# Kernel tuning notes

Measured on AMD Instinct MI355X. Metric: run time of the kernel, lower is better.

Reference implementation:

```python
import jax, jax.numpy as jnp
import numpy as np

NB, DM, DIN, DS, DTR, K = 4, 64, 128, 16, 4, 4
C, COUT, H, W, BATCH, NH = 256, 256, 32, 32, 4, 8


def layernorm(x, w, b, eps=1e-5):
    mu = x.mean(-1, keepdims=True)
    var = ((x - mu) ** 2).mean(-1, keepdims=True)
    return (x - mu) * jax.lax.rsqrt(var + eps) * w + b


def ln_hw(x, eps=1e-5):
    # F.layer_norm(x, [H, W]) -> normalize over last two dims, no affine
    mu = x.mean((-2, -1), keepdims=True)
    var = ((x - mu) ** 2).mean((-2, -1), keepdims=True)
    return (x - mu) * jax.lax.rsqrt(var + eps)


def conv1d(x, w, b, groups=1, pad=1):
    # x: (B, Cin, L), w: (Cout, Cin//groups, k)
    y = jax.lax.conv_general_dilated(x, w, (1,), [(pad, pad)],
                                     dimension_numbers=('NCH', 'OIH', 'NCH'),
                                     feature_group_count=groups)
    return y + b[None, :, None]


def selective_scan(u, dt, Bm, Cm, A, Dp):
    # u, dt: (B,L,din); Bm, Cm: (B,L,ds); A: (din,ds); Dp: (din,)
    dA = jnp.exp(dt[..., None] * A)                     # (B,L,din,ds)
    dBu = (dt * u)[..., None] * Bm[:, :, None, :]       # (B,L,din,ds)

    def step(h, inp):
        dA_t, dBu_t, C_t = inp
        h = dA_t * h + dBu_t
        return h, jnp.einsum('bds,bs->bd', h, C_t)

    h0 = jnp.zeros((u.shape[0], DIN, DS), u.dtype)
    _, ys = jax.lax.scan(step, h0, (dA.transpose(1, 0, 2, 3), dBu.transpose(1, 0, 2, 3), Cm.transpose(1, 0, 2)))
    return ys.transpose(1, 0, 2) + u * Dp


def mamba(xs, inw, convw, convb, xpw, dtw, dtb, alog, dp, outw):
    # xs: (B,L,DM) one branch of Mamba(d_model=DM, d_state=DS, d_conv=K, expand=2)
    xz = xs @ inw.T                                     # (B,L,2*DIN)
    u, z = jnp.split(xz, 2, axis=-1)
    # causal depthwise conv1d (torch pads K-1 and truncates to L == left pad K-1)
    uc = jax.lax.conv_general_dilated(u.transpose(0, 2, 1), convw[:, None, :], (1,), [(K - 1, 0)],
                                      dimension_numbers=('NCH', 'OIH', 'NCH'),
                                      feature_group_count=DIN) + convb[None, :, None]
    u = jax.nn.silu(uc.transpose(0, 2, 1))              # (B,L,DIN)
    xdbc = u @ xpw.T                                    # (B,L,DTR+2*DS)
    dt = jax.nn.softplus(xdbc[..., :DTR] @ dtw.T + dtb)
    Bm, Cm = xdbc[..., DTR:DTR + DS], xdbc[..., DTR + DS:]
    y = selective_scan(u, dt, Bm, Cm, -jnp.exp(alog), dp)
    return (y * jax.nn.silu(z)) @ outw.T


mamba_v = jax.vmap(mamba)  # over branch axis 0 of inputs and all params


def mha(x, inw, inb, outw, outb):
    B, N, Cc = x.shape
    hd = Cc // NH
    qkv = x @ inw.T + inb
    q, k, v = jnp.split(qkv, 3, axis=-1)
    q = q.reshape(B, N, NH, hd).transpose(0, 2, 1, 3)
    k = k.reshape(B, N, NH, hd).transpose(0, 2, 1, 3)
    v = v.reshape(B, N, NH, hd).transpose(0, 2, 1, 3)
    att = jax.nn.softmax((q @ k.transpose(0, 1, 3, 2)) * (1.0 / (hd ** 0.5)), axis=-1)
    o = (att @ v).transpose(0, 2, 1, 3).reshape(B, N, Cc)
    return o @ outw.T + outb


def reference(x, norm_w, norm_b, skip_scale, m_inw, m_convw, m_convb, m_xpw, m_dtw, m_dtb, m_alog, m_d, m_outw, qdw_w, qdw_b, qpw_w, qpw_b, rdw_w, rdw_b, rpw_w, rpw_b, fdw_w, fdw_b, fpw_w, fpw_b, lc_w, lc_b, attn_inw, attn_inb, attn_outw, attn_outb, lgn_w, lgn_b, fc_w, fc_b, dwc_w, dwc_b, proj_w, proj_b):
    B, Cc, Hh, Ww = x.shape
    N = Hh * Ww
    xs = x.reshape(B, Cc, N).transpose(0, 2, 1)         # (B,N,C)
    xn = layernorm(xs, norm_w, norm_b)
    # channel-chunk into NB branches: (NB,B,N,DM)
    xc = xn.reshape(B, N, NB, DM).transpose(2, 0, 1, 3)
    xm = mamba_v(xc, m_inw, m_convw, m_convb, m_xpw, m_dtw, m_dtb, m_alog, m_d, m_outw) + skip_scale * xc
    x_concat = xm.transpose(1, 2, 0, 3).reshape(B, N, Cc)
    # branch gating: depthwise grouped conv (C->NB) then pointwise (NB->NB)
    Q = conv1d(conv1d(x_concat.transpose(0, 2, 1), qdw_w, qdw_b, groups=NB, pad=1), qpw_w, qpw_b, groups=1, pad=0)
    g = jax.nn.sigmoid(Q)                               # (B,NB,N)
    xg = (g.transpose(1, 0, 2)[..., None] * xm).transpose(1, 2, 0, 3).reshape(B, N, Cc)
    xgt = xg.transpose(0, 2, 1)                          # (B,C,N)
    R = conv1d(conv1d(xgt, rdw_w, rdw_b, groups=Cc, pad=1), rpw_w, rpw_b, groups=1, pad=0) + xgt
    cat = jnp.concatenate([xs, R.transpose(0, 2, 1)], axis=-1).transpose(0, 2, 1)  # (B,2C,N)
    xm2 = conv1d(conv1d(cat, fdw_w, fdw_b, groups=2 * Cc, pad=1), fpw_w, fpw_b, groups=1, pad=0) + cat[:, :Cc, :]
    xm2 = xm2.transpose(0, 2, 1)                         # (B,N,C)
    # local-global feature mixing
    x_local = conv1d(xm2.transpose(0, 2, 1), lc_w, lc_b, groups=Cc, pad=1).transpose(0, 2, 1)
    x_global = mha(xm2, attn_inw, attn_inb, attn_outw, attn_outb)
    x_out = jnp.concatenate([x_local, x_global], axis=-1) @ fc_w.T + fc_b
    x_out = jax.nn.gelu(layernorm(x_out, lgn_w, lgn_b), approximate=False)
    # DepthwiseConvolution: layer_norm over [H,W] (no affine) then depthwise conv2d
    xi = x_out.transpose(0, 2, 1).reshape(B, Cc, Hh, Ww)
    xi = ln_hw(xi)
    xi = jax.lax.conv_general_dilated(xi, dwc_w, (1, 1), [(1, 1), (1, 1)],
                                      dimension_numbers=('NCHW', 'OIHW', 'NCHW'),
                                      feature_group_count=Cc) + dwc_b[None, :, None, None]
    x_mixed = xi.reshape(B, Cc, N).transpose(0, 2, 1)
    x_mixed = layernorm(x_mixed, norm_w, norm_b)        # self.norm reused
    x_mixed = x_mixed @ proj_w.T + proj_b
    return x_mixed.transpose(0, 2, 1).reshape(B, COUT, Hh, Ww)


def setup_inputs() -> dict:
    key = jax.random.key(0)
    ks = iter(jax.random.split(key, 64))

    def rn(shape, s=0.02):
        return jax.random.normal(next(ks), shape, jnp.float32) * s

    return dict(
        x=jax.random.normal(next(ks), (BATCH, C, H, W), jnp.float32),
        norm_w=jnp.ones((C,), jnp.float32), norm_b=jnp.zeros((C,), jnp.float32),
        skip_scale=jnp.ones((1,), jnp.float32),
        m_inw=rn((NB, 2 * DIN, DM)), m_convw=rn((NB, DIN, K), 0.2), m_convb=jnp.zeros((NB, DIN), jnp.float32),
        m_xpw=rn((NB, DTR + 2 * DS, DIN)), m_dtw=rn((NB, DIN, DTR), 0.2), m_dtb=rn((NB, DIN), 0.5),
        m_alog=jnp.tile(jnp.log(jnp.arange(1, DS + 1, dtype=jnp.float32)), (NB, DIN, 1)),
        m_d=jnp.ones((NB, DIN), jnp.float32), m_outw=rn((NB, DM, DIN)),
        qdw_w=rn((NB, C // NB, 3), 0.1), qdw_b=jnp.zeros((NB,), jnp.float32),
        qpw_w=rn((NB, NB, 1), 0.3), qpw_b=jnp.zeros((NB,), jnp.float32),
        rdw_w=rn((C, 1, 3), 0.2), rdw_b=jnp.zeros((C,), jnp.float32),
        rpw_w=rn((C, C, 1)), rpw_b=jnp.zeros((C,), jnp.float32),
        fdw_w=rn((2 * C, 1, 3), 0.2), fdw_b=jnp.zeros((2 * C,), jnp.float32),
        fpw_w=rn((C, 2 * C, 1)), fpw_b=jnp.zeros((C,), jnp.float32),
        lc_w=rn((C, 1, 3), 0.2), lc_b=jnp.zeros((C,), jnp.float32),
        attn_inw=rn((3 * C, C)), attn_inb=jnp.zeros((3 * C,), jnp.float32),
        attn_outw=rn((C, C)), attn_outb=jnp.zeros((C,), jnp.float32),
        lgn_w=jnp.ones((C,), jnp.float32), lgn_b=jnp.zeros((C,), jnp.float32),
        fc_w=rn((C, 2 * C)), fc_b=jnp.zeros((C,), jnp.float32),
        dwc_w=rn((C, 1, 3, 3), 0.2), dwc_b=jnp.zeros((C,), jnp.float32),
        proj_w=rn((COUT, C)), proj_b=jnp.zeros((COUT,), jnp.float32),
    )
```

## Files before the change

### kernel.cpp

```cpp
#include <hip/hip_runtime.h>
#include <math.h>


namespace {
constexpr int NB_ = 4, DM_ = 64, DIN_ = 128, DS_ = 16, DTR_ = 4;
constexpr int C_ = 256, N_ = 1024, B_ = 4, HD_ = 32;
constexpr int NCH = 16, LCH = 64;
constexpr int NSTATE = 16 * 128 * 16;
}

typedef __attribute__((ext_vector_type(8))) short bf16x8;
typedef __attribute__((ext_vector_type(4))) float f32x4;
typedef __attribute__((ext_vector_type(8))) unsigned short ushort8v;
typedef __attribute__((ext_vector_type(4))) unsigned short ushort4v;

__device__ __forceinline__ unsigned short f2b(float f) {
  unsigned int u = __float_as_uint(f);
  unsigned int r = u + 0x7FFFu + ((u >> 16) & 1u);
  return (unsigned short)(r >> 16);
}

__device__ __forceinline__ float2 blockReduce2(float a, float b, float* red) {
#pragma unroll
  for (int m = 1; m < 64; m <<= 1) {
// ... 64 lines not shown
__global__ __launch_bounds__(256) void k_inproj_mfma(const float* __restrict__ xn,
                                                     const float* __restrict__ inw,
                                                     float* __restrict__ UPRE,
                                                     float* __restrict__ Z) {
  __shared__ unsigned short xa[64][72];
  __shared__ unsigned short wb[64][72];
  int r0 = blockIdx.x * 64;
  int nb = blockIdx.y >> 2, c0 = (blockIdx.y & 3) * 64;
  int t = threadIdx.x;
  int wv = t >> 6, lane = t & 63, g = lane >> 4, ql = lane & 15;
  const f32x4 zf = {0.f, 0.f, 0.f, 0.f};
  f32x4 acc[4] = {zf, zf, zf, zf};
  int rr = t >> 2, kq = (t & 3) * 16;
  {
    const float* xsrc = xn + (long)(r0 + rr) * C_ + nb * 64 + kq;
#pragma unroll
    for (int j = 0; j < 4; ++j) {
      float4 v = *(const float4*)(xsrc + 4 * j);
      ushort4v u = {f2b(v.x), f2b(v.y), f2b(v.z), f2b(v.w)};
      *(ushort4v*)&xa[rr][kq + 4 * j] = u;
    }
    const float* wsrc = inw + ((long)nb * 256 + c0 + rr) * 64 + kq;
#pragma unroll
    for (int j = 0; j < 4; ++j) {
      float4 v = *(const float4*)(wsrc + 4 * j);
      ushort4v u = {f2b(v.x), f2b(v.y), f2b(v.z), f2b(v.w)};
      *(ushort4v*)&wb[rr][kq + 4 * j] = u;
    }
  }
  __syncthreads();
#pragma unroll
  for (int ks = 0; ks < 2; ++ks) {
    bf16x8 a = *(const bf16x8*)&xa[wv * 16 + ql][ks * 32 + g * 8];
#pragma unroll
    for (int ct = 0; ct < 4; ++ct) {
      bf16x8 b = *(const bf16x8*)&wb[ct * 16 + ql][ks * 32 + g * 8];
      acc[ct] = __builtin_amdgcn_mfma_f32_16x16x32_bf16(a, b, acc[ct], 0, 0, 0);
    }
  }
#pragma unroll
  for (int ct = 0; ct < 4; ++ct) {
    int col = c0 + ct * 16 + ql;
#pragma unroll
    for (int reg = 0; reg < 4; ++reg) {
      long row = (long)nb * 4096 + r0 + wv * 16 + g * 4 + reg;
      if (col < 128) UPRE[row * DIN_ + col] = acc[ct][reg];
      else           Z[row * DIN_ + col - 128] = acc[ct][reg];
    }
  }
}

__global__ __launch_bounds__(256) void k_causal(const float* __restrict__ Uin,
                                                float* __restrict__ Uout,
                                                const float* __restrict__ cw,
                                                const float* __restrict__ cb) {
  __shared__ float u_s[35][128];
  int bx = blockIdx.x;
  int nbb = bx >> 5, chk = bx & 31;
  int nb = nbb >> 2;
  int n0 = chk * 32;
  const float* ibase = Uin + (long)nbb * N_ * DIN_;
  float* obase = Uout + (long)nbb * N_ * DIN_;
  for (int i = threadIdx.x; i < 35 * 32; i += 256) {
    int row = i >> 5, q = i & 31;
    int n = n0 - 3 + row;
    float4 v = (n >= 0) ? *(const float4*)&ibase[(long)n * DIN_ + q * 4]
                        : make_float4(0.f, 0.f, 0.f, 0.f);
    *(float4*)&u_s[row][q * 4] = v;
  }
  __syncthreads();
  int d = threadIdx.x & 127, half = threadIdx.x >> 7;
  float w0 = cw[(nb * DIN_ + d) * 4 + 0], w1 = cw[(nb * DIN_ + d) * 4 + 1];
  float w2 = cw[(nb * DIN_ + d) * 4 + 2], w3 = cw[(nb * DIN_ + d) * 4 + 3];
  float bv = cb[nb * DIN_ + d];
#pragma unroll
  for (int j = 0; j < 16; ++j) {
    int nn = half * 16 + j;
    float acc = bv + w3 * u_s[nn + 3][d] + w2 * u_s[nn + 2][d] +
                w1 * u_s[nn + 1][d] + w0 * u_s[nn][d];
    obase[(long)(n0 + nn) * DIN_ + d] = siluf(acc);
  }
}

__global__ __launch_bounds__(256) void k_xdbc(const float* __restrict__ U,
                                              const float* __restrict__ xpw,
                                              const float* __restrict__ dtw,
                                              const float* __restrict__ dtb,
                                              float* __restrict__ DT,
                                              float* __restrict__ BMb, float* __restrict__ CMb) {
  __shared__ float wl[36][129];
  __shared__ float u16[16][129];
  __shared__ float xd_s[16][37];
  __shared__ float dtw_s[128][4];
  __shared__ float dtb_s[128];
  int t = threadIdx.x;
  long row0 = (long)blockIdx.x * 16;
  int nb = blockIdx.x >> 8;
  for (int i = t; i < 36 * 128; i += 256) wl[i >> 7][i & 127] = xpw[nb * 36 * 128 + i];
  for (int i = t; i < 16 * 128; i += 256) u16[i >> 7][i & 127] = U[(row0 + (i >> 7)) * DIN_ + (i & 127)];
  for (int i = t; i < 512; i += 256) dtw_s[i >> 2][i & 3] = dtw[nb * 512 + i];
  if (t < 128) dtb_s[t] = dtb[nb * DIN_ + t];
  __syncthreads();
  {
    int r = t >> 4, jl = t & 15;
    float a0 = 0.f, a1 = 0.f, a2 = 0.f;
    for (int k = 0; k < 128; ++k) {
      float uv = u16[r][k];
      a0 += uv * wl[jl][k];
      a1 += uv * wl[jl + 16][k];
      if (jl < 4) a2 += uv * wl[jl + 32][k];
    }
    xd_s[r][jl] = a0;
    xd_s[r][jl + 16] = a1;
    if (jl < 4) xd_s[r][jl + 32] = a2;
  }
  __syncthreads();
  {
    int r = t >> 4, s = t & 15;
    BMb[(row0 + r) * DS_ + s] = xd_s[r][4 + s];
    CMb[(row0 + r) * DS_ + s] = xd_s[r][20 + s];
  }
  {
    int r = t >> 4, dl = t & 15;
    float x0 = xd_s[r][0], x1 = xd_s[r][1], x2 = xd_s[r][2], x3 = xd_s[r][3];
#pragma unroll
    for (int dd = 0; dd < 8; ++dd) {
      int d = dl * 8 + dd;
      float a = dtb_s[d] + x0 * dtw_s[d][0] + x1 * dtw_s[d][1] +
                x2 * dtw_s[d][2] + x3 * dtw_s[d][3];
      DT[(row0 + r) * DIN_ + d] = softplusf(a);
    }
  }
}

__global__ __launch_bounds__(256) void k_scanA(const float* __restrict__ DT,
                                               const float* __restrict__ U,
                                               const float* __restrict__ BMb,
                                               const float* __restrict__ alog,
                                               float* __restrict__ Aprod,
                                               float* __restrict__ Hend) {
  __shared__ float dt_s[64][64];
  __shared__ float u_s[64][64];
  __shared__ float bm_s[64][16];
  int bx = blockIdx.x;
  int chunk = bx >> 5, rem = bx & 31, nbb = rem >> 1, dh = rem & 1;
  int nb = nbb >> 2;
  int t = threadIdx.x;
  int dl = t >> 2, sg = t & 3;
  int d = dh * 64 + dl;
  long base = (long)nbb * N_ + chunk * LCH;
#pragma unroll
  for (int j = 0; j < 4; ++j) {
    int f = t + 256 * j;
    int tt = f >> 4, dq = (f & 15) * 4;
    long src = (base + tt) * DIN_ + dh * 64 + dq;
    *(float4*)&dt_s[tt][dq] = *(const float4*)&DT[src];
    *(float4*)&u_s[tt][dq]  = *(const float4*)&U[src];
  }
  {
    int tt = t >> 2, sq = (t & 3) * 4;
    *(float4*)&bm_s[tt][sq] = *(const float4*)&BMb[(base + tt) * DS_ + sq];
  }
  float A[4];
#pragma unroll
  for (int i = 0; i < 4; ++i)
    A[i] = -expf(alog[(nb * DIN_ + d) * DS_ + sg * 4 + i]);
  __syncthreads();
  float h[4] = {0.f, 0.f, 0.f, 0.f};
  float ap[4] = {1.f, 1.f, 1.f, 1.f};
  for (int tt = 0; tt < LCH; ++tt) {
    float dtv = dt_s[tt][dl];
    float uv  = u_s[tt][dl];
    float cc = dtv * uv;
    float4 bm4 = *(const float4*)&bm_s[tt][sg * 4];
    float bmv[4] = {bm4.x, bm4.y, bm4.z, bm4.w};
#pragma unroll
    for (int i = 0; i < 4; ++i) {
      float dA = __expf(dtv * A[i]);
      h[i] = dA * h[i] + cc * bmv[i];
      ap[i] *= dA;
    }
  }
  long st = (long)chunk * NSTATE + ((nbb << 7) + d) * 16 + sg * 4;
  *(float4*)&Aprod[st] = make_float4(ap[0], ap[1], ap[2], ap[3]);
  *(float4*)&Hend[st]  = make_float4(h[0], h[1], h[2], h[3]);
}

__global__ __launch_bounds__(256) void k_scanB(float* __restrict__ Aprod,
                                               const float* __restrict__ Hend) {
  int state = blockIdx.x * 256 + threadIdx.x;
  float H = 0.f;
#pragma unroll
  for (int c = 0; c < NCH; ++c) {
    long idx = (long)c * NSTATE + state;
    float a = Aprod[idx];
    float e = Hend[idx];
    Aprod[idx] = H;
    H = e + a * H;
  }
}

__global__ __launch_bounds__(256) void k_scanC(float* __restrict__ DT,
                                               const float* __restrict__ U,
                                               const float* __restrict__ BMb,
                                               const float* __restrict__ CMb,
                                               const float* __restrict__ alog,
                                               const float* __restrict__ Dp,
                                               const float* __restrict__ Hin) {
  __shared__ float dt_s[64][64];
  __shared__ float u_s[64][64];
  __shared__ float bm_s[64][16];
  __shared__ float cm_s[64][16];
  int bx = blockIdx.x;
// ... 170 lines not shown
  }
}

template <int KD>
__global__ __launch_bounds__(256) void k_gemm_cm_dw(const float* __restrict__ inA,
                                                    const float* __restrict__ inB,
                                                    const float* __restrict__ dww,
                                                    const float* __restrict__ dwb,
                                                    const float* __restrict__ w,
                                                    const float* __restrict__ bias,
                                                    const float* __restrict__ residCM,
                                                    const float* __restrict__ residRM,
                                                    float* __restrict__ outCM,
                                                    float* __restrict__ outRM) {
  __shared__ unsigned short xa[64][72];
  __shared__ unsigned short wb[64][72];
  int rb = blockIdx.x;
  int b = rb >> 4, n0 = (rb & 15) * 64;
  int c0 = blockIdx.y * 64;
  int t = threadIdx.x;
  int wv = t >> 6, lane = t & 63, g = lane >> 4, ql = lane & 15;
  const f32x4 zf = {0.f, 0.f, 0.f, 0.f};
  f32x4 acc[4] = {zf, zf, zf, zf};
  int rr = t >> 2, kq = (t & 3) * 16;
  for (int k0 = 0; k0 < KD; k0 += 64) {
    __syncthreads();
    {
      int k = k0 + rr;
      const float* src = (inB != nullptr && k >= 256)
                             ? inB + ((long)(b * 256 + k - 256)) * 1024
                             : inA + ((long)(b * 256 + k)) * 1024;
      float w0 = dww[k * 3], w1 = dww[k * 3 + 1], w2 = dww[k * 3 + 2], bv = dwb[k];
#pragma unroll
      for (int j = 0; j < 4; ++j) {
        int nb4 = n0 + kq + 4 * j;
        float4 v = *(const float4*)&src[nb4];
        float vm1 = (nb4 > 0) ? src[nb4 - 1] : 0.f;
        float vp4 = (nb4 + 4 < 1024) ? src[nb4 + 4] : 0.f;
        xa[kq + 4 * j + 0][rr] = f2b(bv + w0 * vm1 + w1 * v.x + w2 * v.y);
        xa[kq + 4 * j + 1][rr] = f2b(bv + w0 * v.x + w1 * v.y + w2 * v.z);
        xa[kq + 4 * j + 2][rr] = f2b(bv + w0 * v.y + w1 * v.z + w2 * v.w);
        xa[kq + 4 * j + 3][rr] = f2b(bv + w0 * v.z + w1 * v.w + w2 * vp4);
      }
    }
    const float* wsrc = w + (long)(c0 + rr) * KD + k0 + kq;
#pragma unroll
    for (int j = 0; j < 4; ++j) {
      float4 v = *(const float4*)(wsrc + 4 * j);
      ushort4v u = {f2b(v.x), f2b(v.y), f2b(v.z), f2b(v.w)};
      *(ushort4v*)&wb[rr][kq + 4 * j] = u;
    }
    __syncthreads();
#pragma unroll
    for (int ks = 0; ks < 2; ++ks) {
      bf16x8 a = *(const bf16x8*)&xa[wv * 16 + ql][ks * 32 + g * 8];
#pragma unroll
      for (int ct = 0; ct < 4; ++ct) {
        bf16x8 bfr = *(const bf16x8*)&wb[ct * 16 + ql][ks * 32 + g * 8];
        acc[ct] = __builtin_amdgcn_mfma_f32_16x16x32_bf16(a, bfr, acc[ct], 0, 0, 0);
      }
    }
  }
#pragma unroll
  for (int ct = 0; ct < 4; ++ct) {
    int col = c0 + ct * 16 + ql;
    float bv = bias[col];
    if (outCM) {
      long base = ((long)(b * 256 + col)) * 1024 + n0 + wv * 16 + g * 4;
      float4 r4 = *(const float4*)(residCM + base);
      float4 o = make_float4(acc[ct][0] + bv + r4.x, acc[ct][1] + bv + r4.y,
                             acc[ct][2] + bv + r4.z, acc[ct][3] + bv + r4.w);
      *(float4*)(outCM + base) = o;
    } else {
#pragma unroll
      for (int reg = 0; reg < 4; ++reg) {
        long row = (long)b * 1024 + n0 + wv * 16 + g * 4 + reg;
        long idx = row * 256 + col;
        outRM[idx] = acc[ct][reg] + bv + residRM[idx];
      }
    }
  }
}

template <int KD, bool TOUT>
__global__ __launch_bounds__(256) void k_gemm_rm(const float* __restrict__ inA,
                                                 const float* __restrict__ inB,
                                                 const float* __restrict__ w,
                                                 const float* __restrict__ bias,
                                                 float* __restrict__ out,
                                                 int Cout, int lda) {
  __shared__ unsigned short xa[64][72];
  __shared__ unsigned short wb[64][72];
  __shared__ float tt[TOUT ? 64 : 1][TOUT ? 68 : 1];
  int r0 = blockIdx.x * 64;
  int c0 = blockIdx.y * 64;
  int t = threadIdx.x;
  int wv = t >> 6, lane = t & 63, g = lane >> 4, ql = lane & 15;
  const f32x4 zf = {0.f, 0.f, 0.f, 0.f};
  f32x4 acc[4] = {zf, zf, zf, zf};
  int rr = t >> 2, kq = (t & 3) * 16;
  for (int k0 = 0; k0 < KD; k0 += 64) {
    __syncthreads();
    int kk = k0 + kq;
    const float* xsrc = (inB != nullptr && kk >= KD / 2)
                            ? inB + (long)(r0 + rr) * lda + (kk - KD / 2)
                            : inA + (long)(r0 + rr) * lda + kk;
#pragma unroll
    for (int j = 0; j < 4; ++j) {
      float4 v = *(const float4*)(xsrc + 4 * j);
      ushort4v u = {f2b(v.x), f2b(v.y), f2b(v.z), f2b(v.w)};
      *(ushort4v*)&xa[rr][kq + 4 * j] = u;
    }
    const float* wsrc = w + (long)(c0 + rr) * KD + kk;
#pragma unroll
    for (int j = 0; j < 4; ++j) {
      float4 v = *(const float4*)(wsrc + 4 * j);
      ushort4v u = {f2b(v.x), f2b(v.y), f2b(v.z), f2b(v.w)};
      *(ushort4v*)&wb[rr][kq + 4 * j] = u;
    }
    __syncthreads();
#pragma unroll
    for (int ks = 0; ks < 2; ++ks) {
      bf16x8 a = *(const bf16x8*)&xa[wv * 16 + ql][ks * 32 + g * 8];
#pragma unroll
      for (int ct = 0; ct < 4; ++ct) {
        bf16x8 b = *(const bf16x8*)&wb[ct * 16 + ql][ks * 32 + g * 8];
        acc[ct] = __builtin_amdgcn_mfma_f32_16x16x32_bf16(a, b, acc[ct], 0, 0, 0);
      }
    }
  }
  if constexpr (!TOUT) {
#pragma unroll
    for (int ct = 0; ct < 4; ++ct) {
      int col = c0 + ct * 16 + ql;
      float bv = bias[col];
#pragma unroll
      for (int reg = 0; reg < 4; ++reg) {
        long row = r0 + wv * 16 + g * 4 + reg;
        out[row * Cout + col] = acc[ct][reg] + bv;
      }
    }
  } else {
#pragma unroll
    for (int ct = 0; ct < 4; ++ct) {
      int col = ct * 16 + ql;
      float bv = bias[c0 + col];
#pragma unroll
      for (int reg = 0; reg < 4; ++reg)
        tt[col][wv * 16 + g * 4 + reg] = acc[ct][reg] + bv;
    }
    __syncthreads();
    int b = r0 >> 10, n0 = r0 & 1023;
    int col = t >> 2, nq = (t & 3) * 16;
    float* op = out + ((long)(b * 256 + c0 + col)) * 1024 + n0 + nq;
#pragma unroll
    for (int j = 0; j < 4; ++j) {
      float4 v = make_float4(tt[col][nq + 4 * j], tt[col][nq + 4 * j + 1],
                             tt[col][nq + 4 * j + 2], tt[col][nq + 4 * j + 3]);
      *(float4*)(op + 4 * j) = v;
    }
  }
}

__global__ __launch_bounds__(256) void k_gemm_qkv(const float* __restrict__ in,
                                                  const float* __restrict__ w,
                                                  const float* __restrict__ bias,
                                                  unsigned short* __restrict__ out) {
  __shared__ unsigned short xa[64][72];
  __shared__ unsigned short wb[64][72];
  int r0 = blockIdx.x * 64;
  int c0 = blockIdx.y * 64;
  int t = threadIdx.x;
  int wv = t >> 6, lane = t & 63, g = lane >> 4, ql = lane & 15;
  const f32x4 zf = {0.f, 0.f, 0.f, 0.f};
  f32x4 acc[4] = {zf, zf, zf, zf};
  int rr = t >> 2, kq = (t & 3) * 16;
  for (int k0 = 0; k0 < 256; k0 += 64) {
    __syncthreads();
    const float* xsrc = in + (long)(r0 + rr) * 256 + k0 + kq;
#pragma unroll
    for (int j = 0; j < 4; ++j) {
      float4 v = *(const float4*)(xsrc + 4 * j);
      ushort4v u = {f2b(v.x), f2b(v.y), f2b(v.z), f2b(v.w)};
      *(ushort4v*)&xa[rr][kq + 4 * j] = u;
    }
    const float* wsrc = w + (long)(c0 + rr) * 256 + k0 + kq;
#pragma unroll
    for (int j = 0; j < 4; ++j) {
      float4 v = *(const float4*)(wsrc + 4 * j);
      ushort4v u = {f2b(v.x), f2b(v.y), f2b(v.z), f2b(v.w)};
      *(ushort4v*)&wb[rr][kq + 4 * j] = u;
    }
    __syncthreads();
#pragma unroll
    for (int ks = 0; ks < 2; ++ks) {
      bf16x8 a = *(const bf16x8*)&xa[wv * 16 + ql][ks * 32 + g * 8];
#pragma unroll
      for (int ct = 0; ct < 4; ++ct) {
        bf16x8 b = *(const bf16x8*)&wb[ct * 16 + ql][ks * 32 + g * 8];
        acc[ct] = __builtin_amdgcn_mfma_f32_16x16x32_bf16(a, b, acc[ct], 0, 0, 0);
      }
    }
  }
#pragma unroll
  for (int ct = 0; ct < 4; ++ct) {
    int col = c0 + ct * 16 + ql;
    float bv = bias[col];
#pragma unroll
    for (int reg = 0; reg < 4; ++reg) {
      long row = r0 + wv * 16 + g * 4 + reg;
      out[row * 768 + col] = f2b(acc[ct][reg] + bv);
    }
  }
}

__global__ __launch_bounds__(256) void k_gemm_fc(const float* __restrict__ XM2,
                                                 const float* __restrict__ XGL,
                                                 const float* __restrict__ lcw,
                                                 const float* __restrict__ lcb,
                                                 const float* __restrict__ w,
                                                 const float* __restrict__ bias,
                                                 float* __restrict__ out) {
  __shared__ unsigned short xa[64][72];
  __shared__ unsigned short wb[64][72];
  int r0 = blockIdx.x * 64;
  int c0 = blockIdx.y * 64;
  int t = threadIdx.x;
  int wv = t >> 6, lane = t & 63, g = lane >> 4, ql = lane & 15;
  const f32x4 zf = {0.f, 0.f, 0.f, 0.f};
  f32x4 acc[4] = {zf, zf, zf, zf};
  int rr = t >> 2, kq = (t & 3) * 16;
  for (int k0 = 0; k0 < 512; k0 += 64) {
    __syncthreads();
    int kk = k0 + kq;
    long row = r0 + rr;
    if (kk < 256) {
      int n = (int)(row & 1023);
      const float* pc = XM2 + row * 256 + kk;
      bool hm = n > 0, hp = n < 1023;
#pragma unroll
      for (int j = 0; j < 4; ++j) {
        float4 v = *(const float4*)(pc + 4 * j);
// ... 145 lines not shown
  int b = bx >> 6, n0 = (bx & 63) * 16;
  int c = threadIdx.x;
#pragma unroll
  for (int j = 0; j < 16; ++j)
    tile[c][j] = XO[((long)(b * N_ + n0 + j)) * C_ + c];
  __syncthreads();
  {
    int n = c & 15, g = c >> 4;
    float a = 0.f, q = 0.f;
#pragma unroll
    for (int i = 0; i < 16; ++i) {
      float v = tile[g * 16 + i][n];
      a += v; q += v * v;
    }
    redp[g][n][0] = a; redp[g][n][1] = q;
  }
  __syncthreads();
  if (c < 16) {
    float a = 0.f, q = 0.f;
#pragma unroll
    for (int g2 = 0; g2 < 16; ++g2) { a += redp[g2][c][0]; q += redp[g2][c][1]; }
    float mu = a * (1.f / C_);
    float rs = rsqrtf(q * (1.f / C_) - mu * mu + 1e-5f);
    stats[c][0] = mu; stats[c][1] = rs;
  }
  __syncthreads();
  float wv = lw[c], bv = lb[c];
  float o[16];
#pragma unroll
  for (int j = 0; j < 16; ++j) {
    float x = (tile[c][j] - stats[j][0]) * stats[j][1] * wv + bv;
    o[j] = 0.5f * x * (1.f + erff(x * 0.70710678118654752f));
  }
  float* dst = &XI[((long)(b * C_ + c)) * N_ + n0];
#pragma unroll
  for (int j4 = 0; j4 < 4; ++j4)
    *(float4*)(dst + j4 * 4) = make_float4(o[4 * j4], o[4 * j4 + 1], o[4 * j4 + 2], o[4 * j4 + 3]);
}

__global__ __launch_bounds__(256) void k_lnhw_dwc(const float* __restrict__ XIin,
                                                  const float* __restrict__ w,
                                                  const float* __restrict__ bias,
                                                  float* __restrict__ XD) {
  __shared__ float pl[32][33];
  __shared__ float red[8];
  long base = (long)blockIdx.x * 1024;
  int c = blockIdx.x & 255;
  int t = threadIdx.x;
  float4 v = *(const float4*)&XIin[base + t * 4];
  float a = v.x + v.y + v.z + v.w;
  float q = v.x * v.x + v.y * v.y + v.z * v.z + v.w * v.w;
  float2 s = blockReduce2(a, q, red);
  float mu = s.x * (1.f / 1024.f);
  float rs = rsqrtf(s.y * (1.f / 1024.f) - mu * mu + 1e-5f);
  int hh = t >> 3, w0 = (t & 7) * 4;
  pl[hh][w0 + 0] = (v.x - mu) * rs;
  pl[hh][w0 + 1] = (v.y - mu) * rs;
  pl[hh][w0 + 2] = (v.z - mu) * rs;
  pl[hh][w0 + 3] = (v.w - mu) * rs;
  __syncthreads();
  float wk[9];
#pragma unroll
  for (int i = 0; i < 9; ++i) wk[i] = w[c * 9 + i];
  float bv = bias[c];
  float o[4];
#pragma unroll
  for (int j = 0; j < 4; ++j) {
    int ww = w0 + j;
    float acc = bv;
#pragma unroll
    for (int kh = 0; kh < 3; ++kh) {
      int h2 = hh + kh - 1;
      if (h2 < 0 || h2 >= 32) continue;
#pragma unroll
      for (int kw = 0; kw < 3; ++kw) {
        int w2 = ww + kw - 1;
        if (w2 < 0 || w2 >= 32) continue;
        acc += wk[kh * 3 + kw] * pl[h2][w2];
      }
    }
    o[j] = acc;
  }
  *(float4*)&XD[base + t * 4] = make_float4(o[0], o[1], o[2], o[3]);
}

extern "C" void kernel_launch(void* const* d_in, const int* in_sizes, int n_in,
                              void* d_out, int out_size, void* d_ws, size_t ws_size,
                              hipStream_t stream) {
  const float* x        = (const float*)d_in[0];
  const float* norm_w   = (const float*)d_in[1];
  const float* norm_b   = (const float*)d_in[2];
  const float* skip     = (const float*)d_in[3];
  const float* m_inw    = (const float*)d_in[4];
  const float* m_convw  = (const float*)d_in[5];
  const float* m_convb  = (const float*)d_in[6];
  const float* m_xpw    = (const float*)d_in[7];
  const float* m_dtw    = (const float*)d_in[8];
  const float* m_dtb    = (const float*)d_in[9];
  const float* m_alog   = (const float*)d_in[10];
  const float* m_d      = (const float*)d_in[11];
  const float* m_outw   = (const float*)d_in[12];
  const float* qdw_w    = (const float*)d_in[13];
  const float* qdw_b    = (const float*)d_in[14];
  const float* qpw_w    = (const float*)d_in[15];
  const float* qpw_b    = (const float*)d_in[16];
  const float* rdw_w    = (const float*)d_in[17];
  const float* rdw_b    = (const float*)d_in[18];
  const float* rpw_w    = (const float*)d_in[19];
  const float* rpw_b    = (const float*)d_in[20];
  const float* fdw_w    = (const float*)d_in[21];
  const float* fdw_b    = (const float*)d_in[22];
  const float* fpw_w    = (const float*)d_in[23];
  const float* fpw_b    = (const float*)d_in[24];
  const float* lc_w     = (const float*)d_in[25];
  const float* lc_b     = (const float*)d_in[26];
  const float* attn_inw = (const float*)d_in[27];
  const float* attn_inb = (const float*)d_in[28];
  const float* attn_outw= (const float*)d_in[29];
  const float* attn_outb= (const float*)d_in[30];
  const float* lgn_w    = (const float*)d_in[31];
  const float* lgn_b    = (const float*)d_in[32];
  const float* fc_w     = (const float*)d_in[33];
  const float* fc_b     = (const float*)d_in[34];
  const float* dwc_w    = (const float*)d_in[35];
  const float* dwc_b    = (const float*)d_in[36];
  const float* proj_w   = (const float*)d_in[37];
  const float* proj_b   = (const float*)d_in[38];
  float* out = (float*)d_out;

  float* ws = (float*)d_ws;
  const size_t F = 1048576;
  float* XS  = ws + 0 * F;
  float* XN  = ws + 1 * F;
  float* U   = ws + 2 * F;
  float* Z   = ws + 4 * F;
  float* UPRE= ws + 6 * F;
  float* DT  = ws + 6 * F;
  float* BM  = ws + 8 * F;
  float* CM  = ws + 8 * F + F / 4;
  float* XMC = ws + 8 * F + F / 2;
  float* SC_APROD = ws + 8 * F + F / 2;
  float* SC_HEND  = ws + 9 * F;
  float* G   = ws + 1 * F;
  float* XG  = ws + 2 * F;
  float* RB  = ws + 4 * F;
  float* XM2 = ws + 5 * F;
  unsigned short* QKVB = (unsigned short*)(ws + 1 * F);
  float* O   = ws + 4 * F;
  float* XGL = ws + 6 * F;
  float* XO  = ws + 7 * F;
  float* XI  = ws + 8 * F;
  float* XD  = ws + 5 * F;
  float* LNF = ws + 0 * F;
  (void)ws_size; (void)in_sizes; (void)n_in; (void)out_size;

  k_ln_t2<<<256, 256, 0, stream>>>(x, norm_w, norm_b, XN, XS);
  k_inproj_mfma<<<dim3(64, 16), 256, 0, stream>>>(XN, m_inw, UPRE, Z);
  k_causal<<<512, 256, 0, stream>>>(UPRE, U, m_convw, m_convb);
  k_xdbc<<<1024, 256, 0, stream>>>(U, m_xpw, m_dtw, m_dtb, DT, BM, CM);
  k_scanA<<<512, 256, 0, stream>>>(DT, U, BM, m_alog, SC_APROD, SC_HEND);
  k_scanB<<<128, 256, 0, stream>>>(SC_APROD, SC_HEND);
  k_scanC<<<512, 256, 0, stream>>>(DT, U, BM, CM, m_alog, m_d, SC_APROD);
  k_outproj_mfma<<<dim3(64, 4), 256, 0, stream>>>(DT, Z, m_outw, XN, skip, XMC);
  k_gate<<<256, 256, 0, stream>>>(XMC, qdw_w, qdw_b, qpw_w, qpw_b, G);
  k_xg<<<256, 256, 0, stream>>>(XMC, G, XG);
  k_gemm_cm_dw<256><<<dim3(64, 4), 256, 0, stream>>>(XG, nullptr, rdw_w, rdw_b,
                                                     rpw_w, rpw_b, XG, nullptr, RB, nullptr);
  k_gemm_cm_dw<512><<<dim3(64, 4), 256, 0, stream>>>(x, RB, fdw_w, fdw_b,
                                                     fpw_w, fpw_b, nullptr, XS, nullptr, XM2);
  k_gemm_qkv<<<dim3(64, 12), 256, 0, stream>>>(XM2, attn_inw, attn_inb, QKVB);
  k_attn_mfma<<<512, 256, 0, stream>>>(QKVB, O);
  k_gemm_rm<256, false><<<dim3(64, 4), 256, 0, stream>>>(O, nullptr, attn_outw, attn_outb, XGL, 256, 256);
  k_gemm_fc<<<dim3(64, 4), 256, 0, stream>>>(XM2, XGL, lc_w, lc_b, fc_w, fc_b, XO);
  k_lngelu<<<256, 256, 0, stream>>>(XO, lgn_w, lgn_b, XI);
  k_lnhw_dwc<<<1024, 256, 0, stream>>>(XI, dwc_w, dwc_b, XD);
  k_ln_t2<<<256, 256, 0, stream>>>(XD, norm_w, norm_b, LNF, nullptr);
  k_gemm_rm<256, true><<<dim3(64, 4), 256, 0, stream>>>(LNF, nullptr, proj_w, proj_b, out, 256, 256);
}
```

Baseline: 215.3 us.

## Use MFMA for x_proj GEMM and fuse final layernorm into projection

Replaces the scalar FP32 x_proj kernel with a bf16 MFMA tiled GEMM that handles 64 rows per block and writes its outputs as vector stores. Separately, fuses the final token layernorm into the output projection GEMM: each block computes per-token statistics from the channel-major input and normalizes while staging to LDS. This removes one kernel launch and the round trip of the intermediate LNF buffer through global memory. In exchange, x_proj now runs in bf16, the layernorm statistics are recomputed by each of the four column blocks, and the variance uses the one-pass sum-of-squares form, which can lose precision.

```diff
diff --git a/kernel.cpp b/kernel.cpp
--- a/kernel.cpp
+++ b/kernel.cpp
@@ -170,53 +170,96 @@
   }
 }
 
-__global__ __launch_bounds__(256) void k_xdbc(const float* __restrict__ U,
-                                              const float* __restrict__ xpw,
-                                              const float* __restrict__ dtw,
-                                              const float* __restrict__ dtb,
-                                              float* __restrict__ DT,
-                                              float* __restrict__ BMb, float* __restrict__ CMb) {
-  __shared__ float wl[36][129];
-  __shared__ float u16[16][129];
-  __shared__ float xd_s[16][37];
+__global__ __launch_bounds__(256) void k_xdbc_mfma(const float* __restrict__ U,
+                                                   const float* __restrict__ xpw,
+                                                   const float* __restrict__ dtw,
+                                                   const float* __restrict__ dtb,
+                                                   float* __restrict__ DT,
+                                                   float* __restrict__ BMb,
+                                                   float* __restrict__ CMb) {
+  __shared__ unsigned short xa[64][72];
+  __shared__ unsigned short wb[48][72];
+  __shared__ float xd_s[64][40];
   __shared__ float dtw_s[128][4];
   __shared__ float dtb_s[128];
   int t = threadIdx.x;
-  long row0 = (long)blockIdx.x * 16;
-  int nb = blockIdx.x >> 8;
-  for (int i = t; i < 36 * 128; i += 256) wl[i >> 7][i & 127] = xpw[nb * 36 * 128 + i];
-  for (int i = t; i < 16 * 128; i += 256) u16[i >> 7][i & 127] = U[(row0 + (i >> 7)) * DIN_ + (i & 127)];
+  long row0 = (long)blockIdx.x * 64;
+  int nb = blockIdx.x >> 6;
   for (int i = t; i < 512; i += 256) dtw_s[i >> 2][i & 3] = dtw[nb * 512 + i];
   if (t < 128) dtb_s[t] = dtb[nb * DIN_ + t];
+  int wv = t >> 6, lane = t & 63, g = lane >> 4, ql = lane & 15;
+  const f32x4 zf = {0.f, 0.f, 0.f, 0.f};
+  f32x4 acc[3] = {zf, zf, zf};
+  int rr = t >> 2, kq = (t & 3) * 16;
+  for (int k0 = 0; k0 < 128; k0 += 64) {
+    __syncthreads();
+    const float* xsrc = U + (row0 + rr) * DIN_ + k0 + kq;
+#pragma unroll
+    for (int j = 0; j < 4; ++j) {
+      float4 v = *(const float4*)(xsrc + 4 * j);
+      ushort4v u = {f2b(v.x), f2b(v.y), f2b(v.z), f2b(v.w)};
+      *(ushort4v*)&xa[rr][kq + 4 * j] = u;
+    }
+    if (rr < 48) {
+      if (rr < 36) {
+        const float* wsrc = xpw + (long)nb * 36 * 128 + rr * 128 + k0 + kq;
+#pragma unroll
+        for (int j = 0; j < 4; ++j) {
+          float4 v = *(const float4*)(wsrc + 4 * j);
+          ushort4v u = {f2b(v.x), f2b(v.y), f2b(v.z), f2b(v.w)};
+          *(ushort4v*)&wb[rr][kq + 4 * j] = u;
+        }
+      } else {
+        ushort4v z = {0, 0, 0, 0};
+#pragma unroll
+        for (int j = 0; j < 4; ++j) *(ushort4v*)&wb[rr][kq + 4 * j] = z;
+      }
+    }
+    __syncthreads();
+#pragma unroll
+    for (int ks = 0; ks < 2; ++ks) {
+      bf16x8 a = *(const bf16x8*)&xa[wv * 16 + ql][ks * 32 + g * 8];
+#pragma unroll
+      for (int ct = 0; ct < 3; ++ct) {
+        bf16x8 b = *(const bf16x8*)&wb[ct * 16 + ql][ks * 32 + g * 8];
+        acc[ct] = __builtin_amdgcn_mfma_f32_16x16x32_bf16(a, b, acc[ct], 0, 0, 0);
+      }
+    }
+  }
+#pragma unroll
+  for (int ct = 0; ct < 3; ++ct) {
+    int col = ct * 16 + ql;
+    if (col < 36) {
+#pragma unroll
+      for (int reg = 0; reg < 4; ++reg)
+        xd_s[wv * 16 + g * 4 + reg][col] = acc[ct][reg];
+    }
+  }
   __syncthreads();
   {
-    int r = t >> 4, jl = t & 15;
-    float a0 = 0.f, a1 = 0.f, a2 = 0.f;
-    for (int k = 0; k < 128; ++k) {
-      float uv = u16[r][k];
-      a0 += uv * wl[jl][k];
-      a1 += uv * wl[jl + 16][k];
-      if (jl < 4) a2 += uv * wl[jl + 32][k];
-    }
-    xd_s[r][jl] = a0;
-    xd_s[r][jl + 16] = a1;
-    if (jl < 4) xd_s[r][jl + 32] = a2;
-  }
-  __syncthreads();
+    int r = t >> 2, sq = (t & 3) * 4;
+    float4 bm4 = make_float4(xd_s[r][4 + sq], xd_s[r][5 + sq],
+                             xd_s[r][6 + sq], xd_s[r][7 + sq]);
+    *(float4*)&BMb[(row0 + r) * DS_ + sq] = bm4;
+    float4 cm4 = make_float4(xd_s[r][20 + sq], xd_s[r][21 + sq],
+                             xd_s[r][22 + sq], xd_s[r][23 + sq]);
+    *(float4*)&CMb[(row0 + r) * DS_ + sq] = cm4;
+  }
   {
-    int r = t >> 4, s = t & 15;
-    BMb[(row0 + r) * DS_ + s] = xd_s[r][4 + s];
-    CMb[(row0 + r) * DS_ + s] = xd_s[r][20 + s];
-  }
-  {
-    int r = t >> 4, dl = t & 15;
+    int r = t >> 2, dg = t & 3;
     float x0 = xd_s[r][0], x1 = xd_s[r][1], x2 = xd_s[r][2], x3 = xd_s[r][3];
-#pragma unroll
-    for (int dd = 0; dd < 8; ++dd) {
-      int d = dl * 8 + dd;
-      float a = dtb_s[d] + x0 * dtw_s[d][0] + x1 * dtw_s[d][1] +
-                x2 * dtw_s[d][2] + x3 * dtw_s[d][3];
-      DT[(row0 + r) * DIN_ + d] = softplusf(a);
+    float* dst = DT + (row0 + r) * DIN_ + dg * 32;
+#pragma unroll
+    for (int j = 0; j < 8; ++j) {
+      float o[4];
+#pragma unroll
+      for (int e = 0; e < 4; ++e) {
+        int d = dg * 32 + j * 4 + e;
+        float a = dtb_s[d] + x0 * dtw_s[d][0] + x1 * dtw_s[d][1] +
+                  x2 * dtw_s[d][2] + x3 * dtw_s[d][3];
+        o[e] = softplusf(a);
+      }
+      *(float4*)(dst + j * 4) = make_float4(o[0], o[1], o[2], o[3]);
     }
   }
 }
@@ -553,16 +596,13 @@
   }
 }
 
-template <int KD, bool TOUT>
+template <int KD>
 __global__ __launch_bounds__(256) void k_gemm_rm(const float* __restrict__ inA,
-                                                 const float* __restrict__ inB,
                                                  const float* __restrict__ w,
                                                  const float* __restrict__ bias,
-                                                 float* __restrict__ out,
-                                                 int Cout, int lda) {
+                                                 float* __restrict__ out, int Cout) {
   __shared__ unsigned short xa[64][72];
   __shared__ unsigned short wb[64][72];
-  __shared__ float tt[TOUT ? 64 : 1][TOUT ? 68 : 1];
   int r0 = blockIdx.x * 64;
   int c0 = blockIdx.y * 64;
   int t = threadIdx.x;
@@ -573,9 +613,7 @@
   for (int k0 = 0; k0 < KD; k0 += 64) {
     __syncthreads();
     int kk = k0 + kq;
-    const float* xsrc = (inB != nullptr && kk >= KD / 2)
-                            ? inB + (long)(r0 + rr) * lda + (kk - KD / 2)
-                            : inA + (long)(r0 + rr) * lda + kk;
+    const float* xsrc = inA + (long)(r0 + rr) * KD + kk;
 #pragma unroll
     for (int j = 0; j < 4; ++j) {
       float4 v = *(const float4*)(xsrc + 4 * j);
@@ -600,35 +638,14 @@
       }
     }
   }
-  if constexpr (!TOUT) {
-#pragma unroll
-    for (int ct = 0; ct < 4; ++ct) {
-      int col = c0 + ct * 16 + ql;
-      float bv = bias[col];
-#pragma unroll
-      for (int reg = 0; reg < 4; ++reg) {
-        long row = r0 + wv * 16 + g * 4 + reg;
-        out[row * Cout + col] = acc[ct][reg] + bv;
-      }
-    }
-  } else {
-#pragma unroll
-    for (int ct = 0; ct < 4; ++ct) {
-      int col = ct * 16 + ql;
-      float bv = bias[c0 + col];
-#pragma unroll
-      for (int reg = 0; reg < 4; ++reg)
-        tt[col][wv * 16 + g * 4 + reg] = acc[ct][reg] + bv;
-    }
-    __syncthreads();
-    int b = r0 >> 10, n0 = r0 & 1023;
-    int col = t >> 2, nq = (t & 3) * 16;
-    float* op = out + ((long)(b * 256 + c0 + col)) * 1024 + n0 + nq;
-#pragma unroll
-    for (int j = 0; j < 4; ++j) {
-      float4 v = make_float4(tt[col][nq + 4 * j], tt[col][nq + 4 * j + 1],
-                             tt[col][nq + 4 * j + 2], tt[col][nq + 4 * j + 3]);
-      *(float4*)(op + 4 * j) = v;
+#pragma unroll
+  for (int ct = 0; ct < 4; ++ct) {
+    int col = c0 + ct * 16 + ql;
+    float bv = bias[col];
+#pragma unroll
+    for (int reg = 0; reg < 4; ++reg) {
+      long row = r0 + wv * 16 + g * 4 + reg;
+      out[row * Cout + col] = acc[ct][reg] + bv;
     }
   }
 }
@@ -940,6 +957,86 @@
     o[j] = acc;
   }
   *(float4*)&XD[base + t * 4] = make_float4(o[0], o[1], o[2], o[3]);
+}
+
+__global__ __launch_bounds__(256) void k_lnproj(const float* __restrict__ XD,
+                                                const float* __restrict__ nw,
+                                                const float* __restrict__ nbias,
+                                                const float* __restrict__ w,
+                                                const float* __restrict__ bias,
+                                                float* __restrict__ out) {
+  __shared__ unsigned short xa[64][72];
+  __shared__ unsigned short wb[64][72];
+  __shared__ float ps[4][64], pq[4][64];
+  __shared__ float mu_s[64], rs_s[64];
+  int rb = blockIdx.x;
+  int b = rb >> 4, n0 = (rb & 15) * 64;
+  int c0 = blockIdx.y * 64;
+  int t = threadIdx.x;
+  {
+    int nl = t & 63, cq = t >> 6;
+    const float* src = XD + ((long)(b * 256 + cq * 64)) * 1024 + n0 + nl;
+    float s = 0.f, q = 0.f;
+    for (int i = 0; i < 64; ++i) {
+      float v = src[(long)i * 1024];
+      s += v; q += v * v;
+    }
+    ps[cq][nl] = s; pq[cq][nl] = q;
+  }
+  __syncthreads();
+  if (t < 64) {
+    float s = ps[0][t] + ps[1][t] + ps[2][t] + ps[3][t];
+    float q = pq[0][t] + pq[1][t] + pq[2][t] + pq[3][t];
+    float mu = s * (1.f / 256.f);
+    float rs = rsqrtf(q * (1.f / 256.f) - mu * mu + 1e-5f);
+    mu_s[t] = mu; rs_s[t] = rs;
+  }
+  int wv = t >> 6, lane = t & 63, g = lane >> 4, ql = lane & 15;
+  const f32x4 zf = {0.f, 0.f, 0.f, 0.f};
+  f32x4 acc[4] = {zf, zf, zf, zf};
+  int rr = t >> 2, kq = (t & 3) * 16;
+  for (int k0 = 0; k0 < 256; k0 += 64) {
+    __syncthreads();
+    {
+      int ch = k0 + rr;
+      const float* src = XD + ((long)(b * 256 + ch)) * 1024 + n0 + kq;
+      float wv_ = nw[ch], bv_ = nbias[ch];
+#pragma unroll
+      for (int j = 0; j < 4; ++j) {
+        float4 v = *(const float4*)(src + 4 * j);
+        int n = kq + 4 * j;
+        xa[n + 0][rr] = f2b((v.x - mu_s[n + 0]) * rs_s[n + 0] * wv_ + bv_);
+        xa[n + 1][rr] = f2b((v.y - mu_s[n + 1]) * rs_s[n + 1] * wv_ + bv_);
+        xa[n + 2][rr] = f2b((v.z - mu_s[n + 2]) * rs_s[n + 2] * wv_ + bv_);
+        xa[n + 3][rr] = f2b((v.w - mu_s[n + 3]) * rs_s[n + 3] * wv_ + bv_);
+      }
+      const float* wsrc = w + (long)(c0 + rr) * 256 + k0 + kq;
+#pragma unroll
+      for (int j = 0; j < 4; ++j) {
+        float4 v = *(const float4*)(wsrc + 4 * j);
+        ushort4v u = {f2b(v.x), f2b(v.y), f2b(v.z), f2b(v.w)};
+        *(ushort4v*)&wb[rr][kq + 4 * j] = u;
+      }
+    }
+    __syncthreads();
+#pragma unroll
+    for (int ks = 0; ks < 2; ++ks) {
+      bf16x8 a = *(const bf16x8*)&xa[wv * 16 + ql][ks * 32 + g * 8];
+#pragma unroll
+      for (int ct = 0; ct < 4; ++ct) {
+        bf16x8 bfr = *(const bf16x8*)&wb[ct * 16 + ql][ks * 32 + g * 8];
+        acc[ct] = __builtin_amdgcn_mfma_f32_16x16x32_bf16(a, bfr, acc[ct], 0, 0, 0);
+      }
+    }
+  }
+#pragma unroll
+  for (int ct = 0; ct < 4; ++ct) {
+    int col = c0 + ct * 16 + ql;
+    float bv = bias[col];
+    long basei = ((long)(b * 256 + col)) * 1024 + n0 + wv * 16 + g * 4;
+    *(float4*)(out + basei) = make_float4(acc[ct][0] + bv, acc[ct][1] + bv,
+                                          acc[ct][2] + bv, acc[ct][3] + bv);
+  }
 }
 
 extern "C" void kernel_launch(void* const* d_in, const int* in_sizes, int n_in,
@@ -1009,13 +1106,12 @@
   float* XO  = ws + 7 * F;
   float* XI  = ws + 8 * F;
   float* XD  = ws + 5 * F;
-  float* LNF = ws + 0 * F;
   (void)ws_size; (void)in_sizes; (void)n_in; (void)out_size;
 
   k_ln_t2<<<256, 256, 0, stream>>>(x, norm_w, norm_b, XN, XS);
   k_inproj_mfma<<<dim3(64, 16), 256, 0, stream>>>(XN, m_inw, UPRE, Z);
   k_causal<<<512, 256, 0, stream>>>(UPRE, U, m_convw, m_convb);
-  k_xdbc<<<1024, 256, 0, stream>>>(U, m_xpw, m_dtw, m_dtb, DT, BM, CM);
+  k_xdbc_mfma<<<256, 256, 0, stream>>>(U, m_xpw, m_dtw, m_dtb, DT, BM, CM);
   k_scanA<<<512, 256, 0, stream>>>(DT, U, BM, m_alog, SC_APROD, SC_HEND);
   k_scanB<<<128, 256, 0, stream>>>(SC_APROD, SC_HEND);
   k_scanC<<<512, 256, 0, stream>>>(DT, U, BM, CM, m_alog, m_d, SC_APROD);
@@ -1028,10 +1124,9 @@
                                                      fpw_w, fpw_b, nullptr, XS, nullptr, XM2);
   k_gemm_qkv<<<dim3(64, 12), 256, 0, stream>>>(XM2, attn_inw, attn_inb, QKVB);
   k_attn_mfma<<<512, 256, 0, stream>>>(QKVB, O);
-  k_gemm_rm<256, false><<<dim3(64, 4), 256, 0, stream>>>(O, nullptr, attn_outw, attn_outb, XGL, 256, 256);
+  k_gemm_rm<256><<<dim3(64, 4), 256, 0, stream>>>(O, attn_outw, attn_outb, XGL, 256);
   k_gemm_fc<<<dim3(64, 4), 256, 0, stream>>>(XM2, XGL, lc_w, lc_b, fc_w, fc_b, XO);
   k_lngelu<<<256, 256, 0, stream>>>(XO, lgn_w, lgn_b, XI);
   k_lnhw_dwc<<<1024, 256, 0, stream>>>(XI, dwc_w, dwc_b, XD);
-  k_ln_t2<<<256, 256, 0, stream>>>(XD, norm_w, norm_b, LNF, nullptr);
-  k_gemm_rm<256, true><<<dim3(64, 4), 256, 0, stream>>>(LNF, nullptr, proj_w, proj_b, out, 256, 256);
-}
+  k_lnproj<<<dim3(64, 4), 256, 0, stream>>>(XD, norm_w, norm_b, proj_w, proj_b, out);
+}
```

Measured after the change: 209.3 us. 1.03x faster.
